# Performance work log

Hardware: AMD Instinct MI355X
Metric: run time of the kernel (lower is better)

Reference implementation:

```python
import jax, jax.numpy as jnp
import numpy as np

SCALE = 0.125  # 1/sqrt(d_k), d_k = 64


def setup_inputs() -> dict:
    key = jax.random.key(0)
    kq, kk, kv, kp = jax.random.split(key, 4)
    H, B, L, T, D = 16, 4, 1024, 1024, 64
    return {
        "query": jax.random.normal(kq, (H, B, L, D), dtype=jnp.float32),
        "key": jax.random.normal(kk, (H, B, T, D), dtype=jnp.float32),
        "value": jax.random.normal(kv, (H, B, T, D), dtype=jnp.float32),
        "prev_attention": jax.random.normal(kp, (H, B, L, T), dtype=jnp.float32),
    }


def reference(query, key, value, prev_attention):
    # scores: [h, b, l, t]
    scores = jnp.einsum("hblk,hbtk->hblt", query, key) * SCALE
    scores = scores + prev_attention
    attention = jax.nn.softmax(scores, axis=-1)
    # dropout disabled (rate 0.0) for deterministic reference
    output = jnp.einsum("hblt,hbtv->hblv", attention, value)
    return (output, attention)
```

## Files before the change

kernel.cpp:

```cpp
#include <hip/hip_runtime.h>

#define SCALE 0.125f

constexpr int L_ = 1024, T_ = 1024, D_ = 64, HB_ = 64, QB = 16;

using f32x4 = __attribute__((ext_vector_type(4))) float;
using half8 = __attribute__((ext_vector_type(8))) _Float16;
using half4 = __attribute__((ext_vector_type(4))) _Float16;

__global__ __launch_bounds__(256, 3) void attn_fused(
    const float* __restrict__ q, const float* __restrict__ kk,
    const float* __restrict__ vv, const float* __restrict__ prev,
    float* __restrict__ out, float* __restrict__ att) {
  __shared__ __align__(16) _Float16 El[QB][1032];
  __shared__ __align__(16) unsigned char KV[18432];
  __shared__ float zb[4][16];

  auto Ks  = (_Float16(*)[72])KV;
  auto Vt  = (_Float16(*)[72])(KV + 9216);
  auto ob4 = (float(*)[16][72])KV;

  const int ltile = blockIdx.x;
  const int hb    = blockIdx.y;
  const int tid = threadIdx.x;
  const int w = tid >> 6, l = tid & 63, l15 = l & 15, lg = l >> 4;
  const int qrow = ltile * QB + l15;

  half8 qb2[2];
  {
    const float* qp = q + ((size_t)hb * L_ + qrow) * D_ + lg * 8;
#pragma unroll
    for (int f = 0; f < 2; ++f)
#pragma unroll
      for (int e = 0; e < 8; ++e) qb2[f][e] = (_Float16)qp[f * 32 + e];
  }

  const float* prow =
      prev + ((size_t)hb * L_ + qrow) * (size_t)T_ + w * 16 + lg * 4;
  const float* kbase = kk + (size_t)hb * T_ * D_;
  const float* vbase = vv + (size_t)hb * T_ * D_;

  const int sr = tid >> 2;
  const int sc = (tid & 3) * 16;
  const int dj = (tid & 3) * 4;

  float4 kq[2][4], vq[2][4];
  f32x4 pbv[2];
  auto kload = [&](int c, int s) {
    const float* p = kbase + (size_t)(c * 64 + sr) * D_ + sc;
#pragma unroll
    for (int i = 0; i < 4; ++i) kq[s][i] = *(const float4*)(p + i * 4);
  };
  auto vload = [&](int c, int s) {
    const float* p = vbase + (size_t)(c * 64 + sr) * D_;
#pragma unroll
    for (int i = 0; i < 4; ++i) vq[s][i] = *(const float4*)(p + i * 16 + dj);
  };
  auto pload = [&](int c, int s) { pbv[s] = *(const f32x4*)(prow + c * 64); };
  auto kwrite = [&](int s) {
    half8 h0, h1;
    const float* f0 = (const float*)&kq[s][0];
    const float* f1 = (const float*)&kq[s][2];
#pragma unroll
    for (int e = 0; e < 8; ++e) {
      h0[e] = (_Float16)f0[e];
      h1[e] = (_Float16)f1[e];
    }
    *(half8*)&Ks[sr][sc] = h0;
    *(half8*)&Ks[sr][sc + 8] = h1;
  };
  auto vwrite = [&](int s) {
#pragma unroll
    for (int i = 0; i < 4; ++i) {
      Vt[i * 16 + dj + 0][sr] = (_Float16)vq[s][i].x;
      Vt[i * 16 + dj + 1][sr] = (_Float16)vq[s][i].y;
      Vt[i * 16 + dj + 2][sr] = (_Float16)vq[s][i].z;
      Vt[i * 16 + dj + 3][sr] = (_Float16)vq[s][i].w;
    }
  };

  kload(0, 0); vload(0, 0); pload(0, 0);
  kwrite(0); vwrite(0);
  kload(1, 1); vload(1, 1); pload(1, 1);

  float zsum = 0.f;
  f32x4 oacc[4];
#pragma unroll
  for (int nd = 0; nd < 4; ++nd) oacc[nd] = (f32x4){0.f, 0.f, 0.f, 0.f};

#pragma unroll 2
  for (int c = 0; c < 16; ++c) {
    __syncthreads();
    f32x4 pv = pbv[c & 1];
    if (c < 14) {
      kload(c + 2, c & 1);
      vload(c + 2, c & 1);
      pload(c + 2, c & 1);
    }

    const int trow = w * 16 + l15;
    half8 ka0 = *(const half8*)&Ks[trow][lg * 8];
    half8 ka1 = *(const half8*)&Ks[trow][32 + lg * 8];
    f32x4 acc = {0.f, 0.f, 0.f, 0.f};
    acc = __builtin_amdgcn_mfma_f32_16x16x32_f16(ka0, qb2[0], acc, 0, 0, 0);
    acc = __builtin_amdgcn_mfma_f32_16x16x32_f16(ka1, qb2[1], acc, 0, 0, 0);

    float e0 = __expf(acc[0] * SCALE + pv[0]);
    float e1 = __expf(acc[1] * SCALE + pv[1]);
    float e2 = __expf(acc[2] * SCALE + pv[2]);
    float e3 = __expf(acc[3] * SCALE + pv[3]);
    zsum += (e0 + e1) + (e2 + e3);
    half4 ev;
    ev[0] = (_Float16)e0; ev[1] = (_Float16)e1;
    ev[2] = (_Float16)e2; ev[3] = (_Float16)e3;
    *(half4*)&El[l15][c * 64 + w * 16 + lg * 4] = ev;

    half8 af;
    af[0] = ev[0]; af[1] = ev[1]; af[2] = ev[2]; af[3] = ev[3];
    af[4] = af[5] = af[6] = af[7] = (_Float16)0.f;
#pragma unroll
    for (int nd = 0; nd < 4; ++nd) {
      half4 v4 = *(const half4*)&Vt[nd * 16 + l15][w * 16 + lg * 4];
      half8 vb;
      vb[0] = v4[0]; vb[1] = v4[1]; vb[2] = v4[2]; vb[3] = v4[3];
      vb[4] = vb[5] = vb[6] = vb[7] = (_Float16)0.f;
      oacc[nd] = __builtin_amdgcn_mfma_f32_16x16x32_f16(af, vb, oacc[nd], 0, 0, 0);
    }

    __syncthreads();
    if (c < 15) { kwrite((c + 1) & 1); vwrite((c + 1) & 1); }
  }

  zsum += __shfl_xor(zsum, 16, 64);
  zsum += __shfl_xor(zsum, 32, 64);
  if (lg == 0) zb[w][l15] = zsum;

#pragma unroll
  for (int nd = 0; nd < 4; ++nd)
#pragma unroll
    for (int i = 0; i < 4; ++i)
      ob4[w][lg * 4 + i][nd * 16 + l15] = oacc[nd][i];
  __syncthreads();

  {
    const int qq = tid >> 4, dd = (tid & 15) * 4;
    const float z =
        (zb[0][qq] + zb[1][qq]) + (zb[2][qq] + zb[3][qq]);
    const float rzq = 1.0f / z;
    f32x4 o0 = *(const f32x4*)&ob4[0][qq][dd];
    f32x4 o1 = *(const f32x4*)&ob4[1][qq][dd];
    f32x4 o2 = *(const f32x4*)&ob4[2][qq][dd];
    f32x4 o3 = *(const f32x4*)&ob4[3][qq][dd];
    f32x4 o = ((o0 + o1) + (o2 + o3));
    o[0] *= rzq; o[1] *= rzq; o[2] *= rzq; o[3] *= rzq;
    *(f32x4*)(out + ((size_t)hb * L_ + ltile * QB + qq) * (size_t)D_ + dd) = o;
  }

  {
    const int row = tid >> 4, tc = tid & 15;
    const float z =
        (zb[0][row] + zb[1][row]) + (zb[2][row] + zb[3][row]);
    const float rzr = 1.0f / z;
    float* attw =
        att + ((size_t)hb * L_ + ltile * QB + row) * (size_t)T_ + tc * 4;
    const _Float16* ep = &El[row][tc * 4];
#pragma unroll
    for (int j = 0; j < 16; ++j) {
      half4 ev = *(const half4*)(ep + j * 64);
      f32x4 s = {(float)ev[0] * rzr, (float)ev[1] * rzr,
                 (float)ev[2] * rzr, (float)ev[3] * rzr};
      *(f32x4*)(attw + j * 64) = s;
    }
  }
}

extern "C" void kernel_launch(void* const* d_in, const int* in_sizes, int n_in,
                              void* d_out, int out_size, void* d_ws,
                              size_t ws_size, hipStream_t stream) {
  const float* q    = (const float*)d_in[0];
  const float* k    = (const float*)d_in[1];
  const float* v    = (const float*)d_in[2];
  const float* prev = (const float*)d_in[3];

  float* out = (float*)d_out;
  float* att = out + (size_t)HB_ * L_ * D_;

  dim3 grid(L_ / QB, HB_);
  attn_fused<<<grid, 256, 0, stream>>>(q, k, v, prev, out, att);
}
```

Before: 250.4 us.

## Remap V staging to packed half2 transposed stores, lighter barriers, MFMA priority

Each thread now loads a 4x4 patch of V (four t-rows by four d-columns) instead of one t-row, so the transposed shared-memory write becomes packed half2 stores rather than scalar 16-bit stores. This cuts the number of LDS write instructions and likely bank conflicts in the transpose. The __syncthreads calls become a raw s_waitcnt lgkmcnt(0) plus s_barrier, which does not wait for outstanding global loads, so prefetches can stay in flight across the barrier. The compute section is wrapped in s_setprio to favour MFMA issue. The inline-asm barrier relies on the compiler not reordering memory accesses across it.

After: 248.5 us. About the same (-0.8%).

```diff
diff --git a/kernel.cpp b/kernel.cpp
--- a/kernel.cpp
+++ b/kernel.cpp
@@ -4,9 +4,12 @@
 
 constexpr int L_ = 1024, T_ = 1024, D_ = 64, HB_ = 64, QB = 16;
 
-using f32x4 = __attribute__((ext_vector_type(4))) float;
-using half8 = __attribute__((ext_vector_type(8))) _Float16;
-using half4 = __attribute__((ext_vector_type(4))) _Float16;
+using f32x4  = __attribute__((ext_vector_type(4))) float;
+using half8  = __attribute__((ext_vector_type(8))) _Float16;
+using half4  = __attribute__((ext_vector_type(4))) _Float16;
+using half2v = __attribute__((ext_vector_type(2))) _Float16;
+
+#define BARRIER() asm volatile("s_waitcnt lgkmcnt(0)\n\ts_barrier" ::: "memory")
 
 __global__ __launch_bounds__(256, 3) void attn_fused(
     const float* __restrict__ q, const float* __restrict__ kk,
@@ -42,40 +45,42 @@
 
   const int sr = tid >> 2;
   const int sc = (tid & 3) * 16;
-  const int dj = (tid & 3) * 4;
+  const int sv_d = (tid & 15) * 4;
+  const int sv_t = (tid >> 4) * 4;
 
-  float4 kq[2][4], vq[2][4];
+  f32x4 kq[2][4], vq[2][4];
   f32x4 pbv[2];
   auto kload = [&](int c, int s) {
     const float* p = kbase + (size_t)(c * 64 + sr) * D_ + sc;
 #pragma unroll
-    for (int i = 0; i < 4; ++i) kq[s][i] = *(const float4*)(p + i * 4);
+    for (int i = 0; i < 4; ++i) kq[s][i] = *(const f32x4*)(p + i * 4);
   };
   auto vload = [&](int c, int s) {
-    const float* p = vbase + (size_t)(c * 64 + sr) * D_;
+    const float* p = vbase + (size_t)(c * 64 + sv_t) * D_ + sv_d;
 #pragma unroll
-    for (int i = 0; i < 4; ++i) vq[s][i] = *(const float4*)(p + i * 16 + dj);
+    for (int j = 0; j < 4; ++j) vq[s][j] = *(const f32x4*)(p + j * D_);
   };
   auto pload = [&](int c, int s) { pbv[s] = *(const f32x4*)(prow + c * 64); };
   auto kwrite = [&](int s) {
     half8 h0, h1;
-    const float* f0 = (const float*)&kq[s][0];
-    const float* f1 = (const float*)&kq[s][2];
 #pragma unroll
-    for (int e = 0; e < 8; ++e) {
-      h0[e] = (_Float16)f0[e];
-      h1[e] = (_Float16)f1[e];
+    for (int e = 0; e < 4; ++e) {
+      h0[e]     = (_Float16)kq[s][0][e];
+      h0[4 + e] = (_Float16)kq[s][1][e];
+      h1[e]     = (_Float16)kq[s][2][e];
+      h1[4 + e] = (_Float16)kq[s][3][e];
     }
     *(half8*)&Ks[sr][sc] = h0;
     *(half8*)&Ks[sr][sc + 8] = h1;
   };
   auto vwrite = [&](int s) {
 #pragma unroll
-    for (int i = 0; i < 4; ++i) {
-      Vt[i * 16 + dj + 0][sr] = (_Float16)vq[s][i].x;
-      Vt[i * 16 + dj + 1][sr] = (_Float16)vq[s][i].y;
-      Vt[i * 16 + dj + 2][sr] = (_Float16)vq[s][i].z;
-      Vt[i * 16 + dj + 3][sr] = (_Float16)vq[s][i].w;
+    for (int dd = 0; dd < 4; ++dd) {
+      half2v a, b;
+      a[0] = (_Float16)vq[s][0][dd]; a[1] = (_Float16)vq[s][1][dd];
+      b[0] = (_Float16)vq[s][2][dd]; b[1] = (_Float16)vq[s][3][dd];
+      *(half2v*)&Vt[sv_d + dd][sv_t]     = a;
+      *(half2v*)&Vt[sv_d + dd][sv_t + 2] = b;
     }
   };
 
@@ -90,7 +95,7 @@
 
 #pragma unroll 2
   for (int c = 0; c < 16; ++c) {
-    __syncthreads();
+    BARRIER();
     f32x4 pv = pbv[c & 1];
     if (c < 14) {
       kload(c + 2, c & 1);
@@ -98,6 +103,7 @@
       pload(c + 2, c & 1);
     }
 
+    __builtin_amdgcn_s_setprio(1);
     const int trow = w * 16 + l15;
     half8 ka0 = *(const half8*)&Ks[trow][lg * 8];
     half8 ka1 = *(const half8*)&Ks[trow][32 + lg * 8];
@@ -126,8 +132,9 @@
       vb[4] = vb[5] = vb[6] = vb[7] = (_Float16)0.f;
       oacc[nd] = __builtin_amdgcn_mfma_f32_16x16x32_f16(af, vb, oacc[nd], 0, 0, 0);
     }
+    __builtin_amdgcn_s_setprio(0);
 
-    __syncthreads();
+    BARRIER();
     if (c < 15) { kwrite((c + 1) & 1); vwrite((c + 1) & 1); }
   }
 
@@ -144,8 +151,7 @@
 
   {
     const int qq = tid >> 4, dd = (tid & 15) * 4;
-    const float z =
-        (zb[0][qq] + zb[1][qq]) + (zb[2][qq] + zb[3][qq]);
+    const float z = (zb[0][qq] + zb[1][qq]) + (zb[2][qq] + zb[3][qq]);
     const float rzq = 1.0f / z;
     f32x4 o0 = *(const f32x4*)&ob4[0][qq][dd];
     f32x4 o1 = *(const f32x4*)&ob4[1][qq][dd];
@@ -158,8 +164,7 @@
 
   {
     const int row = tid >> 4, tc = tid & 15;
-    const float z =
-        (zb[0][row] + zb[1][row]) + (zb[2][row] + zb[3][row]);
+    const float z = (zb[0][row] + zb[1][row]) + (zb[2][row] + zb[3][row]);
     const float rzr = 1.0f / z;
     float* attw =
         att + ((size_t)hb * L_ + ltile * QB + row) * (size_t)T_ + tc * 4;
```
